# Kernel tuning notes

Hardware: AMD Instinct MI355X
Metric: run time of the kernel (lower is better)

Reference implementation:

```python
import jax, jax.numpy as jnp
import numpy as np

S, C, L, B, K, N = 1000, 100, 50, 20, 64, 16384


def setup_inputs() -> dict:
    key = jax.random.key(0)
    ks = jax.random.split(key, 6)
    return {
        "X": jax.random.uniform(ks[0], (N, L), dtype=jnp.float32),
        "stu": jax.random.randint(ks[1], (N,), 0, S),
        "cour": jax.random.randint(ks[2], (N,), 0, C),
        "csa": jax.random.normal(ks[3], (S, C, L, B), dtype=jnp.float32),
        "P": jax.random.normal(ks[4], (K, C), dtype=jnp.float32),
        "D": jax.random.normal(ks[5], (K, B), dtype=jnp.float32),
        "P_A": jnp.ones((K, C), jnp.float32),
        "P_B": jnp.zeros((K, C), jnp.float32),
        "P_C": jax.random.uniform(jax.random.fold_in(key, 7), (B, B), dtype=jnp.float32),
        "D_A": jnp.ones((K, B), jnp.float32),
        "D_B": jnp.zeros((K, B), jnp.float32),
        "guess_": jnp.full((1, C), -2.0, jnp.float32),
        "slide_": jnp.full((1, C), -2.0, jnp.float32),
    }


def reference(X, stu, cour, csa, P, D, P_A, P_B, P_C, D_A, D_B, guess_, slide_):
    # Q-matrix from softmax-normalized P ([K,C], rows over courses) and D ([K,B], cols over concepts)
    Pm = jax.nn.softmax(P * P_A + P_B, axis=1)          # [K, C]
    Dm = jax.nn.softmax(D * D_A + D_B, axis=0)          # [K, B]
    Q = Pm.T @ (Dm @ P_C)                               # [C, B]
    # Batched version of the per-sample python loop: gather + softmax(dim=0) + matvec
    csa_sel = jax.nn.softmax(csa[stu, cour], axis=1)    # [N, L, B], softmax over L
    A = jnp.einsum('nl,nlb->nb', X, csa_sel)            # [N, B]
    Y_ = A @ Q.T                                        # [N, C]
    slide = jax.nn.sigmoid(slide_)
    guess = jax.nn.sigmoid(guess_)
    return (1.0 - slide) * Y_ + guess * (1.0 - Y_)
```

## Files before the change

### kernel.cpp

```cpp
#include <hip/hip_runtime.h>
#include <hip/hip_bf16.h>
#include <math.h>

#define CC 100
#define LL 50
#define BB 20
#define KK 64

__global__ __launch_bounds__(256) void compute_q_kernel(
    const float* __restrict__ P, const float* __restrict__ D,
    const float* __restrict__ P_A, const float* __restrict__ P_B,
    const float* __restrict__ P_C, const float* __restrict__ D_A,
    const float* __restrict__ D_B, const float* __restrict__ guess_,
    const float* __restrict__ slide_,
    float* __restrict__ Q2, float* __restrict__ G)
{
    __shared__ float Pm[KK * CC];
    __shared__ float Dm[KK * BB];
    __shared__ float E [KK * BB];
    __shared__ float PCs[BB * BB];
    __shared__ float scale[CC];
    const int t = threadIdx.x;

    for (int i = t; i < KK * CC; i += 256) Pm[i] = fmaf(P[i], P_A[i], P_B[i]);
    for (int i = t; i < KK * BB; i += 256) Dm[i] = fmaf(D[i], D_A[i], D_B[i]);
    for (int i = t; i < BB * BB; i += 256) PCs[i] = P_C[i];
    if (t < CC) {
        const float g  = 1.f / (1.f + __expf(-guess_[t]));
        const float sl = 1.f / (1.f + __expf(-slide_[t]));
        scale[t] = 1.f - sl - g;
        G[t] = g;
    }
    __syncthreads();

    {
        const int r = t >> 2, q = t & 3;
        float* row = Pm + r * CC + q * 25;
        float m = -INFINITY;
        #pragma unroll
        for (int i = 0; i < 25; ++i) m = fmaxf(m, row[i]);
        m = fmaxf(m, __shfl_xor(m, 1));
        m = fmaxf(m, __shfl_xor(m, 2));
        float s = 0.f;
        #pragma unroll
        for (int i = 0; i < 25; ++i) { float e = __expf(row[i] - m); row[i] = e; s += e; }
        s += __shfl_xor(s, 1);
        s += __shfl_xor(s, 2);
        const float inv = 1.f / s;
        #pragma unroll
        for (int i = 0; i < 25; ++i) row[i] *= inv;
    }
    if (t < 4 * BB) {
        const int b = t >> 2, q = t & 3;
        float m = -INFINITY;
        #pragma unroll
        for (int k = q * 16; k < q * 16 + 16; ++k) m = fmaxf(m, Dm[k * BB + b]);
        m = fmaxf(m, __shfl_xor(m, 1));
        m = fmaxf(m, __shfl_xor(m, 2));
        float s = 0.f;
        #pragma unroll
        for (int k = q * 16; k < q * 16 + 16; ++k) { float e = __expf(Dm[k * BB + b] - m); Dm[k * BB + b] = e; s += e; }
        s += __shfl_xor(s, 1);
        s += __shfl_xor(s, 2);
        const float inv = 1.f / s;
        #pragma unroll
        for (int k = q * 16; k < q * 16 + 16; ++k) Dm[k * BB + b] *= inv;
    }
    __syncthreads();

    for (int i = t; i < KK * BB; i += 256) {
        const int k = i / BB, b = i % BB;
        float acc = 0.f;
        #pragma unroll
        for (int j = 0; j < BB; ++j) acc = fmaf(Dm[k * BB + j], PCs[j * BB + b], acc);
        E[i] = acc;
    }
    __syncthreads();

    for (int i = t; i < CC * BB; i += 256) {
        const int c = i / BB, b = i % BB;
        float acc = 0.f;
        #pragma unroll
        for (int k = 0; k < KK; ++k) acc = fmaf(Pm[k * CC + c], E[k * BB + b], acc);
        Q2[i] = acc * scale[c];
    }
}

__global__ __launch_bounds__(256) void main_kernel(
    const float* __restrict__ X, const int* __restrict__ stu,
    const int* __restrict__ cour, const float* __restrict__ csa,
    const float* __restrict__ Q2, const float* __restrict__ G,
    float* __restrict__ out, int N)
{
    __shared__ __align__(16) float V[4][LL * BB];
    __shared__ float Xs[4][LL];
    const int t = threadIdx.x;
    const int w = t >> 6, lane = t & 63;
    const int n = blockIdx.x * 4 + w;
    if (n >= N) return;

    const int s = stu[n], c = cour[n];
    const float4* __restrict__ src4 =
        (const float4*)(csa + ((size_t)s * CC + c) * (size_t)(LL * BB));
    float4* V4 = (float4*)V[w];

    #pragma unroll
    for (int r = 0; r < 4; ++r) {
        const int idx = r * 64 + lane;
        if (idx < (LL * BB) / 4) V4[idx] = src4[idx];
    }
    if (lane < LL) Xs[w][lane] = X[(size_t)n * LL + lane];

    asm volatile("s_waitcnt lgkmcnt(0)" ::: "memory");
    __builtin_amdgcn_sched_barrier(0);

    const int b = lane % BB;
    const int g = lane / BB;
    float ssum = 0.f, tsum = 0.f;
    if (g < 3) {
        const int l0 = (g == 0) ? 0 : (g == 1) ? 17 : 34;
        const int l1 = (g == 0) ? 17 : (g == 1) ? 34 : LL;
        for (int l = l0; l < l1; ++l) {
            const float e = __expf(V[w][l * BB + b]);
            ssum += e;
            tsum = fmaf(e, Xs[w][l], tsum);
        }
    }
    const float sT = __shfl(ssum, b) + __shfl(ssum, b + BB) + __shfl(ssum, b + 2 * BB);
    const float tT = __shfl(tsum, b) + __shfl(tsum, b + BB) + __shfl(tsum, b + 2 * BB);
    const float Aval = tT / sT;

    float4 q0[5], q1[5];
    const float4* Q2v0 = (const float4*)(Q2 + lane * BB);
    #pragma unroll
    for (int k = 0; k < 5; ++k) q0[k] = Q2v0[k];
    if (lane < CC - 64) {
        const float4* Q2v1 = (const float4*)(Q2 + (64 + lane) * BB);
        #pragma unroll
        for (int k = 0; k < 5; ++k) q1[k] = Q2v1[k];
    }
    float y0 = 0.f, y1 = 0.f;
    #pragma unroll
    for (int bb = 0; bb < BB; ++bb) {
        const float a = __shfl(Aval, bb);
        y0 = fmaf(a, ((const float*)q0)[bb], y0);
        y1 = fmaf(a, ((const float*)q1)[bb], y1);
    }
    float* orow = out + (size_t)n * CC;
    orow[lane] = y0 + G[lane];
    if (lane < CC - 64) orow[64 + lane] = y1 + G[64 + lane];
}

extern "C" void kernel_launch(void* const* d_in, const int* in_sizes, int n_in,
                              void* d_out, int out_size, void* d_ws, size_t ws_size,
                              hipStream_t stream) {
    const float* X      = (const float*)d_in[0];
    const int*   stu    = (const int*)  d_in[1];
    const int*   cour   = (const int*)  d_in[2];
    const float* csa    = (const float*)d_in[3];
    const float* P      = (const float*)d_in[4];
    const float* D      = (const float*)d_in[5];
    const float* P_A    = (const float*)d_in[6];
    const float* P_B    = (const float*)d_in[7];
    const float* P_C    = (const float*)d_in[8];
    const float* D_A    = (const float*)d_in[9];
    const float* D_B    = (const float*)d_in[10];
    const float* guess_ = (const float*)d_in[11];
    const float* slide_ = (const float*)d_in[12];
    float* out = (float*)d_out;
    float* Q2  = (float*)d_ws;
    float* G   = (float*)d_ws + CC * BB;

    const int N = in_sizes[1];

    compute_q_kernel<<<1, 256, 0, stream>>>(P, D, P_A, P_B, P_C, D_A, D_B,
                                            guess_, slide_, Q2, G);
    main_kernel<<<(N + 3) / 4, 256, 0, stream>>>(X, stu, cour, csa, Q2, G, out, N);
}
```

Measured before the change: 36.41 us.

## Load csa rows directly into registers, hoist Q2 loads, use readlane broadcasts

The main kernel stops staging each gathered csa slice and X row in LDS. Each lane now loads its 16–17 strided elements straight into registers, and the Q2 and G loads are hoisted above the softmax so their latency overlaps the gather. Shuffles used as broadcasts become readlane, and compute_q now uses float4 loads plus a register-blocked Q product. Per-lane strided 4-byte global loads replace coalesced float4 copies, which may reduce memory efficiency, and lanes 60–63 redundantly reload rows.

```diff
diff --git a/kernel.cpp b/kernel.cpp
--- a/kernel.cpp
+++ b/kernel.cpp
@@ -22,9 +22,33 @@
     __shared__ float scale[CC];
     const int t = threadIdx.x;
 
-    for (int i = t; i < KK * CC; i += 256) Pm[i] = fmaf(P[i], P_A[i], P_B[i]);
-    for (int i = t; i < KK * BB; i += 256) Dm[i] = fmaf(D[i], D_A[i], D_B[i]);
-    for (int i = t; i < BB * BB; i += 256) PCs[i] = P_C[i];
+    {
+        const float4* P4  = (const float4*)P;
+        const float4* PA4 = (const float4*)P_A;
+        const float4* PB4 = (const float4*)P_B;
+        float4* Pm4 = (float4*)Pm;
+        for (int i = t; i < (KK * CC) / 4; i += 256) {
+            const float4 p = P4[i], a = PA4[i], bb = PB4[i];
+            float4 r;
+            r.x = fmaf(p.x, a.x, bb.x); r.y = fmaf(p.y, a.y, bb.y);
+            r.z = fmaf(p.z, a.z, bb.z); r.w = fmaf(p.w, a.w, bb.w);
+            Pm4[i] = r;
+        }
+        const float4* D4  = (const float4*)D;
+        const float4* DA4 = (const float4*)D_A;
+        const float4* DB4 = (const float4*)D_B;
+        float4* Dm4 = (float4*)Dm;
+        for (int i = t; i < (KK * BB) / 4; i += 256) {
+            const float4 p = D4[i], a = DA4[i], bb = DB4[i];
+            float4 r;
+            r.x = fmaf(p.x, a.x, bb.x); r.y = fmaf(p.y, a.y, bb.y);
+            r.z = fmaf(p.z, a.z, bb.z); r.w = fmaf(p.w, a.w, bb.w);
+            Dm4[i] = r;
+        }
+        const float4* PC4 = (const float4*)P_C;
+        float4* PCs4 = (float4*)PCs;
+        for (int i = t; i < (BB * BB) / 4; i += 256) PCs4[i] = PC4[i];
+    }
     if (t < CC) {
         const float g  = 1.f / (1.f + __expf(-guess_[t]));
         const float sl = 1.f / (1.f + __expf(-slide_[t]));
@@ -77,12 +101,28 @@
     }
     __syncthreads();
 
-    for (int i = t; i < CC * BB; i += 256) {
-        const int c = i / BB, b = i % BB;
-        float acc = 0.f;
-        #pragma unroll
-        for (int k = 0; k < KK; ++k) acc = fmaf(Pm[k * CC + c], E[k * BB + b], acc);
-        Q2[i] = acc * scale[c];
+    if (t < 128) {
+        const int w = t >> 6, lane = t & 63;
+        const int craw = w * 50 + lane;
+        const int c = craw < CC ? craw : CC - 1;
+        float acc[BB];
+        #pragma unroll
+        for (int j = 0; j < BB; ++j) acc[j] = 0.f;
+        for (int k = 0; k < KK; ++k) {
+            const float pm = Pm[k * CC + c];
+            const float ev = E[k * BB + (lane % BB)];
+            #pragma unroll
+            for (int j = 0; j < BB; ++j) {
+                const float ej = __uint_as_float(
+                    __builtin_amdgcn_readlane(__float_as_uint(ev), j));
+                acc[j] = fmaf(pm, ej, acc[j]);
+            }
+        }
+        if (craw < CC) {
+            const float sc = scale[c];
+            #pragma unroll
+            for (int j = 0; j < BB; ++j) Q2[c * BB + j] = acc[j] * sc;
+        }
     }
 }
 
@@ -92,63 +132,75 @@
     const float* __restrict__ Q2, const float* __restrict__ G,
     float* __restrict__ out, int N)
 {
-    __shared__ __align__(16) float V[4][LL * BB];
-    __shared__ float Xs[4][LL];
     const int t = threadIdx.x;
     const int w = t >> 6, lane = t & 63;
     const int n = blockIdx.x * 4 + w;
     if (n >= N) return;
 
     const int s = stu[n], c = cour[n];
-    const float4* __restrict__ src4 =
-        (const float4*)(csa + ((size_t)s * CC + c) * (size_t)(LL * BB));
-    float4* V4 = (float4*)V[w];
-
-    #pragma unroll
-    for (int r = 0; r < 4; ++r) {
-        const int idx = r * 64 + lane;
-        if (idx < (LL * BB) / 4) V4[idx] = src4[idx];
-    }
-    if (lane < LL) Xs[w][lane] = X[(size_t)n * LL + lane];
-
-    asm volatile("s_waitcnt lgkmcnt(0)" ::: "memory");
-    __builtin_amdgcn_sched_barrier(0);
+    const float* __restrict__ base = csa + ((size_t)s * CC + c) * (size_t)(LL * BB);
+    const float* __restrict__ xrow = X + (size_t)n * LL;
 
     const int b = lane % BB;
     const int g = lane / BB;
+    const int l0 = (g >= 3) ? 0 : g * 17;
+    const bool has17 = (g != 2);
+
+    const int c1ok = (lane < CC - 64);
+    float4 q0[5], q1[5];
+    {
+        const float4* Q2v0 = (const float4*)(Q2 + lane * BB);
+        #pragma unroll
+        for (int k = 0; k < 5; ++k) q0[k] = Q2v0[k];
+        if (c1ok) {
+            const float4* Q2v1 = (const float4*)(Q2 + (64 + lane) * BB);
+            #pragma unroll
+            for (int k = 0; k < 5; ++k) q1[k] = Q2v1[k];
+        }
+    }
+    const float g0v = G[lane];
+    const float g1v = c1ok ? G[64 + lane] : 0.f;
+
+    float vbuf[16], xbuf[16];
+    #pragma unroll
+    for (int i = 0; i < 16; ++i) {
+        vbuf[i] = base[(l0 + i) * BB + b];
+        xbuf[i] = xrow[l0 + i];
+    }
+    float v16 = 0.f, x16 = 0.f;
+    if (has17) {
+        v16 = base[(l0 + 16) * BB + b];
+        x16 = xrow[l0 + 16];
+    }
+
     float ssum = 0.f, tsum = 0.f;
-    if (g < 3) {
-        const int l0 = (g == 0) ? 0 : (g == 1) ? 17 : 34;
-        const int l1 = (g == 0) ? 17 : (g == 1) ? 34 : LL;
-        for (int l = l0; l < l1; ++l) {
-            const float e = __expf(V[w][l * BB + b]);
-            ssum += e;
-            tsum = fmaf(e, Xs[w][l], tsum);
-        }
-    }
+    #pragma unroll
+    for (int i = 0; i < 16; ++i) {
+        const float e = __expf(vbuf[i]);
+        ssum += e;
+        tsum = fmaf(e, xbuf[i], tsum);
+    }
+    if (has17) {
+        const float e = __expf(v16);
+        ssum += e;
+        tsum = fmaf(e, x16, tsum);
+    }
+
     const float sT = __shfl(ssum, b) + __shfl(ssum, b + BB) + __shfl(ssum, b + 2 * BB);
     const float tT = __shfl(tsum, b) + __shfl(tsum, b + BB) + __shfl(tsum, b + 2 * BB);
     const float Aval = tT / sT;
 
-    float4 q0[5], q1[5];
-    const float4* Q2v0 = (const float4*)(Q2 + lane * BB);
-    #pragma unroll
-    for (int k = 0; k < 5; ++k) q0[k] = Q2v0[k];
-    if (lane < CC - 64) {
-        const float4* Q2v1 = (const float4*)(Q2 + (64 + lane) * BB);
-        #pragma unroll
-        for (int k = 0; k < 5; ++k) q1[k] = Q2v1[k];
-    }
     float y0 = 0.f, y1 = 0.f;
     #pragma unroll
     for (int bb = 0; bb < BB; ++bb) {
-        const float a = __shfl(Aval, bb);
+        const float a = __uint_as_float(
+            __builtin_amdgcn_readlane(__float_as_uint(Aval), bb));
         y0 = fmaf(a, ((const float*)q0)[bb], y0);
         y1 = fmaf(a, ((const float*)q1)[bb], y1);
     }
     float* orow = out + (size_t)n * CC;
-    orow[lane] = y0 + G[lane];
-    if (lane < CC - 64) orow[64 + lane] = y1 + G[64 + lane];
+    orow[lane] = y0 + g0v;
+    if (c1ok) orow[64 + lane] = y1 + g1v;
 }
 
 extern "C" void kernel_launch(void* const* d_in, const int* in_sizes, int n_in,
```

Result: faster. 33.46 us (-8.1%).

## Parallelize Q computation across courses and drop LDS staging in main kernel

Applied to the files above, without the earlier changes.

The Q-matrix kernel now launches one block per course instead of a single block. Each block recomputes the P row sums and the D column softmax in registers, then reduces with wave shuffles to produce its own Q row. The main kernel loads csa values straight into registers instead of staging them through shared memory, broadcasts X with shuffles, and hoists the Q2 and G loads ahead of the exp loop. The softmax max-subtraction is removed, which risks overflow for large logits, and the P/D work is repeated in every block.

```diff
diff --git a/kernel.cpp b/kernel.cpp
--- a/kernel.cpp
+++ b/kernel.cpp
@@ -15,74 +15,80 @@
     const float* __restrict__ slide_,
     float* __restrict__ Q2, float* __restrict__ G)
 {
-    __shared__ float Pm[KK * CC];
-    __shared__ float Dm[KK * BB];
-    __shared__ float E [KK * BB];
+    const int c    = blockIdx.x;
+    const int t    = threadIdx.x;
+    const int w    = t >> 6;
+    const int lane = t & 63;
+
     __shared__ float PCs[BB * BB];
-    __shared__ float scale[CC];
-    const int t = threadIdx.x;
+    __shared__ float rowsum_sh[KK];
 
-    for (int i = t; i < KK * CC; i += 256) Pm[i] = fmaf(P[i], P_A[i], P_B[i]);
-    for (int i = t; i < KK * BB; i += 256) Dm[i] = fmaf(D[i], D_A[i], D_B[i]);
-    for (int i = t; i < BB * BB; i += 256) PCs[i] = P_C[i];
-    if (t < CC) {
-        const float g  = 1.f / (1.f + __expf(-guess_[t]));
-        const float sl = 1.f / (1.f + __expf(-slide_[t]));
-        scale[t] = 1.f - sl - g;
-        G[t] = g;
+    if (t < (BB * BB) / 4) ((float4*)PCs)[t] = ((const float4*)P_C)[t];
+
+    {
+        const int k = t >> 2, q = t & 3;
+        const float* __restrict__ pr  = P   + k * CC + q * 25;
+        const float* __restrict__ par = P_A + k * CC + q * 25;
+        const float* __restrict__ pbr = P_B + k * CC + q * 25;
+        float s = 0.f;
+        #pragma unroll
+        for (int i = 0; i < 25; ++i) s += __expf(fmaf(pr[i], par[i], pbr[i]));
+        s += __shfl_xor(s, 1);
+        s += __shfl_xor(s, 2);
+        if (q == 0) rowsum_sh[k] = s;
+    }
+
+    float dm[BB];
+    {
+        const float4* d4  = (const float4*)(D   + lane * BB);
+        const float4* da4 = (const float4*)(D_A + lane * BB);
+        const float4* db4 = (const float4*)(D_B + lane * BB);
+        #pragma unroll
+        for (int i = 0; i < 5; ++i) {
+            const float4 dv = d4[i], av = da4[i], bv = db4[i];
+            dm[4 * i + 0] = __expf(fmaf(dv.x, av.x, bv.x));
+            dm[4 * i + 1] = __expf(fmaf(dv.y, av.y, bv.y));
+            dm[4 * i + 2] = __expf(fmaf(dv.z, av.z, bv.z));
+            dm[4 * i + 3] = __expf(fmaf(dv.w, av.w, bv.w));
+        }
+    }
+    #pragma unroll
+    for (int b = 0; b < BB; ++b) {
+        float s = dm[b];
+        s += __shfl_xor(s, 1);  s += __shfl_xor(s, 2);  s += __shfl_xor(s, 4);
+        s += __shfl_xor(s, 8);  s += __shfl_xor(s, 16); s += __shfl_xor(s, 32);
+        dm[b] *= (1.f / s);
     }
     __syncthreads();
 
-    {
-        const int r = t >> 2, q = t & 3;
-        float* row = Pm + r * CC + q * 25;
-        float m = -INFINITY;
-        #pragma unroll
-        for (int i = 0; i < 25; ++i) m = fmaxf(m, row[i]);
-        m = fmaxf(m, __shfl_xor(m, 1));
-        m = fmaxf(m, __shfl_xor(m, 2));
-        float s = 0.f;
-        #pragma unroll
-        for (int i = 0; i < 25; ++i) { float e = __expf(row[i] - m); row[i] = e; s += e; }
-        s += __shfl_xor(s, 1);
-        s += __shfl_xor(s, 2);
-        const float inv = 1.f / s;
-        #pragma unroll
-        for (int i = 0; i < 25; ++i) row[i] *= inv;
-    }
-    if (t < 4 * BB) {
-        const int b = t >> 2, q = t & 3;
-        float m = -INFINITY;
-        #pragma unroll
-        for (int k = q * 16; k < q * 16 + 16; ++k) m = fmaxf(m, Dm[k * BB + b]);
-        m = fmaxf(m, __shfl_xor(m, 1));
-        m = fmaxf(m, __shfl_xor(m, 2));
-        float s = 0.f;
-        #pragma unroll
-        for (int k = q * 16; k < q * 16 + 16; ++k) { float e = __expf(Dm[k * BB + b] - m); Dm[k * BB + b] = e; s += e; }
-        s += __shfl_xor(s, 1);
-        s += __shfl_xor(s, 2);
-        const float inv = 1.f / s;
-        #pragma unroll
-        for (int k = q * 16; k < q * 16 + 16; ++k) Dm[k * BB + b] *= inv;
-    }
-    __syncthreads();
-
-    for (int i = t; i < KK * BB; i += 256) {
-        const int k = i / BB, b = i % BB;
+    float ev[5];
+    #pragma unroll
+    for (int j = 0; j < 5; ++j) {
+        const int b = 5 * w + j;
         float acc = 0.f;
         #pragma unroll
-        for (int j = 0; j < BB; ++j) acc = fmaf(Dm[k * BB + j], PCs[j * BB + b], acc);
-        E[i] = acc;
+        for (int jj = 0; jj < BB; ++jj) acc = fmaf(dm[jj], PCs[jj * BB + b], acc);
+        ev[j] = acc;
     }
-    __syncthreads();
 
-    for (int i = t; i < CC * BB; i += 256) {
-        const int c = i / BB, b = i % BB;
-        float acc = 0.f;
+    const float ps = fmaf(P[lane * CC + c], P_A[lane * CC + c], P_B[lane * CC + c]);
+    const float pm = __expf(ps) / rowsum_sh[lane];
+
+    float qv[5];
+    #pragma unroll
+    for (int j = 0; j < 5; ++j) {
+        float v = pm * ev[j];
+        v += __shfl_xor(v, 1);  v += __shfl_xor(v, 2);  v += __shfl_xor(v, 4);
+        v += __shfl_xor(v, 8);  v += __shfl_xor(v, 16); v += __shfl_xor(v, 32);
+        qv[j] = v;
+    }
+    if (lane == 0) {
+        const float g  = 1.f / (1.f + __expf(-guess_[c]));
+        const float sl = 1.f / (1.f + __expf(-slide_[c]));
+        const float scale = 1.f - sl - g;
         #pragma unroll
-        for (int k = 0; k < KK; ++k) acc = fmaf(Pm[k * CC + c], E[k * BB + b], acc);
-        Q2[i] = acc * scale[c];
+        for (int j = 0; j < 5; ++j) Q2[c * BB + 5 * w + j] = qv[j] * scale;
+        if (w == 0) G[c] = g;
     }
 }
 
@@ -92,63 +98,70 @@
     const float* __restrict__ Q2, const float* __restrict__ G,
     float* __restrict__ out, int N)
 {
-    __shared__ __align__(16) float V[4][LL * BB];
-    __shared__ float Xs[4][LL];
     const int t = threadIdx.x;
     const int w = t >> 6, lane = t & 63;
     const int n = blockIdx.x * 4 + w;
     if (n >= N) return;
 
     const int s = stu[n], c = cour[n];
-    const float4* __restrict__ src4 =
-        (const float4*)(csa + ((size_t)s * CC + c) * (size_t)(LL * BB));
-    float4* V4 = (float4*)V[w];
-
-    #pragma unroll
-    for (int r = 0; r < 4; ++r) {
-        const int idx = r * 64 + lane;
-        if (idx < (LL * BB) / 4) V4[idx] = src4[idx];
-    }
-    if (lane < LL) Xs[w][lane] = X[(size_t)n * LL + lane];
-
-    asm volatile("s_waitcnt lgkmcnt(0)" ::: "memory");
-    __builtin_amdgcn_sched_barrier(0);
+    const float* __restrict__ base = csa + ((size_t)s * CC + c) * (size_t)(LL * BB);
 
     const int b = lane % BB;
     const int g = lane / BB;
-    float ssum = 0.f, tsum = 0.f;
-    if (g < 3) {
-        const int l0 = (g == 0) ? 0 : (g == 1) ? 17 : 34;
-        const int l1 = (g == 0) ? 17 : (g == 1) ? 34 : LL;
-        for (int l = l0; l < l1; ++l) {
-            const float e = __expf(V[w][l * BB + b]);
-            ssum += e;
-            tsum = fmaf(e, Xs[w][l], tsum);
+    const int l0 = (g >= 3) ? 0 : g * 17;
+    const bool has17 = (g != 2);
+
+    float vbuf[16];
+    #pragma unroll
+    for (int i = 0; i < 16; ++i) vbuf[i] = base[(l0 + i) * BB + b];
+    float v16 = 0.f;
+    if (has17) v16 = base[(l0 + 16) * BB + b];
+
+    const float xv = (lane < LL) ? X[(size_t)n * LL + lane] : 0.f;
+
+    const int c1ok = (lane < CC - 64);
+    float4 q0[5], q1[5];
+    {
+        const float4* Q2v0 = (const float4*)(Q2 + lane * BB);
+        #pragma unroll
+        for (int k = 0; k < 5; ++k) q0[k] = Q2v0[k];
+        if (c1ok) {
+            const float4* Q2v1 = (const float4*)(Q2 + (64 + lane) * BB);
+            #pragma unroll
+            for (int k = 0; k < 5; ++k) q1[k] = Q2v1[k];
         }
     }
+    const float g0v = G[lane];
+    const float g1v = c1ok ? G[64 + lane] : 0.f;
+
+    float ssum = 0.f, tsum = 0.f;
+    #pragma unroll
+    for (int i = 0; i < 16; ++i) {
+        const float e = __expf(vbuf[i]);
+        ssum += e;
+        tsum = fmaf(e, __shfl(xv, l0 + i), tsum);
+    }
+    if (has17) {
+        const float e = __expf(v16);
+        ssum += e;
+        tsum = fmaf(e, __shfl(xv, l0 + 16), tsum);
+    }
+
     const float sT = __shfl(ssum, b) + __shfl(ssum, b + BB) + __shfl(ssum, b + 2 * BB);
     const float tT = __shfl(tsum, b) + __shfl(tsum, b + BB) + __shfl(tsum, b + 2 * BB);
     const float Aval = tT / sT;
 
-    float4 q0[5], q1[5];
-    const float4* Q2v0 = (const float4*)(Q2 + lane * BB);
-    #pragma unroll
-    for (int k = 0; k < 5; ++k) q0[k] = Q2v0[k];
-    if (lane < CC - 64) {
-        const float4* Q2v1 = (const float4*)(Q2 + (64 + lane) * BB);
-        #pragma unroll
-        for (int k = 0; k < 5; ++k) q1[k] = Q2v1[k];
-    }
     float y0 = 0.f, y1 = 0.f;
     #pragma unroll
     for (int bb = 0; bb < BB; ++bb) {
-        const float a = __shfl(Aval, bb);
+        const float a = __uint_as_float(
+            __builtin_amdgcn_readlane(__float_as_uint(Aval), bb));
         y0 = fmaf(a, ((const float*)q0)[bb], y0);
         y1 = fmaf(a, ((const float*)q1)[bb], y1);
     }
     float* orow = out + (size_t)n * CC;
-    orow[lane] = y0 + G[lane];
-    if (lane < CC - 64) orow[64 + lane] = y1 + G[64 + lane];
+    orow[lane] = y0 + g0v;
+    if (c1ok) orow[64 + lane] = y1 + g1v;
 }
 
 extern "C" void kernel_launch(void* const* d_in, const int* in_sizes, int n_in,
@@ -173,7 +186,7 @@
 
     const int N = in_sizes[1];
 
-    compute_q_kernel<<<1, 256, 0, stream>>>(P, D, P_A, P_B, P_C, D_A, D_B,
-                                            guess_, slide_, Q2, G);
+    compute_q_kernel<<<CC, 256, 0, stream>>>(P, D, P_A, P_B, P_C, D_A, D_B,
+                                             guess_, slide_, Q2, G);
     main_kernel<<<(N + 3) / 4, 256, 0, stream>>>(X, stu, cour, csa, Q2, G, out, N);
 }
```

New measurement: 32.64 us. 10.3% less time.
